# Kernel tuning notes

Hardware: AMD Instinct MI355X
Metric: run time of the kernel (lower is better)

## Reference

```python
import jax, jax.numpy as jnp
import numpy as np

BITS = (2, 4, 8)
GROUP = 4
EPS = 1e-5


def _ste_round(x):
    return x + jax.lax.stop_gradient(jnp.round(x) - x)


def _quant_act(x, b):
    s = float(2 ** b - 1)
    return _ste_round(jnp.clip(x, 0.0, 1.0) * s) / s


def _quant_weight(w, mean, std, b):
    # normalize by (mean, std) of the gating-selected channels, then b-bit uniform quant on [-1, 1]
    wn = jnp.clip((w - mean) / (std + EPS), -1.0, 1.0)
    s = float(2 ** b - 1)
    u = _ste_round((wn + 1.0) * 0.5 * s) / s
    return 2.0 * u - 1.0


def _mixed_qconv(x, w, w_mean, w_std, w_logits, a_logits):
    # bitwidth-selectable conv: softmax mixture over quantized weights / activations
    pw = jax.nn.softmax(w_logits)
    pa = jax.nn.softmax(a_logits)
    w_mix = sum(pw[i] * _quant_weight(w, w_mean, w_std, b) for i, b in enumerate(BITS))
    x_mix = sum(pa[i] * _quant_act(x, b) for i, b in enumerate(BITS))
    return jax.lax.conv_general_dilated(
        x_mix, w_mix, window_strides=(1, 1), padding='SAME',
        dimension_numbers=('NCHW', 'OIHW', 'NCHW'))


def _bn(x, g, b, m, v):
    inv = jax.lax.rsqrt(v + EPS)
    return (x - m[None, :, None, None]) * (g * inv)[None, :, None, None] + b[None, :, None, None]


def _masked_mean_std(w, mask):
    # mean/std over gate-selected filter slices; torch uses .data -> stop_gradient, unbiased std
    m = jnp.broadcast_to(mask, w.shape)
    cnt = jnp.sum(m)
    mean = jnp.sum(w * m) / cnt
    var = jnp.sum(m * (w - mean) ** 2) / (cnt - 1.0)
    return jax.lax.stop_gradient(mean), jax.lax.stop_gradient(jnp.sqrt(var))


def _indicator(w1, thr):
    n, c, h, wk = w1.shape
    fw = w1.reshape(n // GROUP, GROUP * c * h * wk)
    nf = fw / jnp.max(jnp.abs(fw))
    norm = jnp.sum(jnp.abs(nf), axis=1) / (GROUP * c * h * wk)  # [n_choices]
    soft = jax.nn.sigmoid(norm - thr)
    hard = (norm > thr).astype(w1.dtype)
    return hard - jax.lax.stop_gradient(soft) + soft  # STE indicator


def setup_inputs() -> dict:
    key = jax.random.key(0)
    ks = jax.random.split(key, 10)
    B, C, H, W = 64, 256, 32, 32
    return {
        'x': jax.random.normal(ks[0], (B, C, H, W), jnp.float32),
        'w1': jax.random.normal(ks[1], (C, C, 3, 3), jnp.float32) * 0.05,
        'w2': jax.random.normal(ks[2], (C, C, 3, 3), jnp.float32) * 0.05,
        'bn1_gamma': jnp.ones((C,), jnp.float32),
        'bn1_beta': jnp.zeros((C,), jnp.float32),
        'bn1_mean': jax.random.normal(ks[3], (C,), jnp.float32) * 0.1,
        'bn1_var': jax.random.uniform(ks[4], (C,), jnp.float32, 0.5, 1.5),
        'bn2_gamma': jnp.ones((C,), jnp.float32),
        'bn2_beta': jnp.zeros((C,), jnp.float32),
        'bn2_mean': jax.random.normal(ks[5], (C,), jnp.float32) * 0.1,
        'bn2_var': jax.random.uniform(ks[6], (C,), jnp.float32, 0.5, 1.5),
        'threshold': jnp.zeros((1,), jnp.float32),
        'w_logits1': jax.random.normal(ks[7], (3,), jnp.float32) * 0.1,
        'a_logits1': jax.random.normal(ks[8], (3,), jnp.float32) * 0.1,
        'w_logits2': jax.random.normal(ks[9], (3,), jnp.float32) * 0.1,
        'a_logits2': jnp.zeros((3,), jnp.float32),
    }


def reference(x, w1, w2, bn1_gamma, bn1_beta, bn1_mean, bn1_var,
              bn2_gamma, bn2_beta, bn2_mean, bn2_var, threshold,
              w_logits1, a_logits1, w_logits2, a_logits2):
    thr = threshold[0]
    ind = _indicator(w1, thr)                       # [n_choices]
    ind_ch = jnp.repeat(ind, GROUP)                 # [out_plane]
    gate_mask = jax.lax.stop_gradient((ind_ch > 0).astype(x.dtype))

    # both_preact path
    residual = x
    h = jax.nn.relu(_bn(x, bn1_gamma, bn1_beta, bn1_mean, bn1_var))
    m1, s1 = _masked_mean_std(w1, gate_mask[:, None, None, None])
    h = _mixed_qconv(h, w1, m1, s1, w_logits1, a_logits1)
    h = jax.nn.relu(_bn(h, bn2_gamma, bn2_beta, bn2_mean, bn2_var))
    m2, s2 = _masked_mean_std(w2, gate_mask[None, :, None, None])
    h = h * ind_ch[None, :, None, None]             # differentiable channel gating
    h = _mixed_qconv(h, w2, m2, s2, w_logits2, a_logits2)
    return h + residual
```

## Files before the change

kernel.cpp:

```cpp
#include <hip/hip_runtime.h>
#include <stdint.h>

#define EPSF 1e-5f

typedef _Float16 h8_t __attribute__((ext_vector_type(8)));
typedef float f4_t __attribute__((ext_vector_type(4)));

#define BB 64
#define CC 256
#define HH 32
#define WW 32
#define HP 34
#define WP 34
#define MTOT (BB*HH*WW)
#define WELEMS (CC*CC*9)
#define PADIMG (HP*WP*CC)
#define PADTOT (BB*PADIMG)

#define S_MAXABS 0
#define S_GSUM   1
#define S_SUM1   129
#define S_SQ1    130
#define S_SUM2   131
#define S_SQ2    132
#define S_M1     133
#define S_S1     134
#define S_M2     135
#define S_S2     136
#define S_PW1    137
#define S_PA1    140
#define S_PW2    143
#define S_PA2    146
#define S_INDCH  160
#define S_GATE   416
#define S_BN1SC  672
#define S_BN1SH  928
#define S_BN2SC  1184
#define S_BN2SH  1440

#define OFF_STATS 0
#define OFF_A1    8192
#define OFF_A2    (OFF_A1 + PADTOT*2)
#define OFF_W1T   (OFF_A2 + PADTOT*2)
#define OFF_W2T   (OFF_W1T + 9*CC*CC*2)

__device__ __forceinline__ void async_load16(void* lds, const void* g) {
  __builtin_amdgcn_global_load_lds(
      reinterpret_cast<uint32_t __attribute__((address_space(1)))*>((uintptr_t)g),
      reinterpret_cast<uint32_t __attribute__((address_space(3)))*>((uint32_t)(uintptr_t)lds),
      16, 0, 0);
}

__device__ __forceinline__ float wave_sum(float v) {
  for (int o = 32; o; o >>= 1) v += __shfl_down(v, o);
  return v;
}
__device__ __forceinline__ float wave_max(float v) {
  for (int o = 32; o; o >>= 1) v = fmaxf(v, __shfl_down(v, o));
  return v;
}

__global__ void k_groupstats(const float* __restrict__ w1, float* stats) {
  int g = blockIdx.x;
  const float* p = w1 + g * 9216;
  float s = 0.f, mx = 0.f;
  for (int i = threadIdx.x; i < 9216; i += 256) {
    float v = fabsf(p[i]);
    s += v; mx = fmaxf(mx, v);
  }
  s = wave_sum(s); mx = wave_max(mx);
  __shared__ float ls[4], lm[4];
  int lane = threadIdx.x & 63, w = threadIdx.x >> 6;
  if (lane == 0) { ls[w] = s; lm[w] = mx; }
  __syncthreads();
  if (threadIdx.x == 0) {
    float ss = ls[0] + ls[1] + ls[2] + ls[3];
    float mm = fmaxf(fmaxf(lm[0], lm[1]), fmaxf(lm[2], lm[3]));
    stats[S_GSUM + g] = ss;
    atomicMax((unsigned int*)(stats + S_MAXABS), __float_as_uint(mm));
  }
}

__device__ __forceinline__ void softmax3(const float* l, float* out) {
  float m = fmaxf(fmaxf(l[0], l[1]), l[2]);
  float e0 = expf(l[0] - m), e1 = expf(l[1] - m), e2 = expf(l[2] - m);
  float inv = 1.f / (e0 + e1 + e2);
  out[0] = e0 * inv; out[1] = e1 * inv; out[2] = e2 * inv;
}

__global__ void k_prep(const float* thr_p,
                       const float* bn1g, const float* bn1b, const float* bn1m, const float* bn1v,
                       const float* bn2g, const float* bn2b, const float* bn2m, const float* bn2v,
                       const float* wl1, const float* al1, const float* wl2, const float* al2,
                       float* stats) {
  int t = threadIdx.x;
  float thr = thr_p[0];
  float maxab = stats[S_MAXABS];
  __shared__ float ind[64];
  if (t < 64) {
    float norm = stats[S_GSUM + t] / maxab / 9216.0f;
    float soft = 1.f / (1.f + expf(-(norm - thr)));
    float hard = (norm > thr) ? 1.f : 0.f;
    ind[t] = (hard - soft) + soft;
  }
  __syncthreads();
  {
    float iv = ind[t >> 2];
    stats[S_INDCH + t] = iv;
    stats[S_GATE + t] = (iv > 0.f) ? 1.f : 0.f;
    float sc1 = bn1g[t] * (1.f / sqrtf(bn1v[t] + EPSF));
    stats[S_BN1SC + t] = sc1;
    stats[S_BN1SH + t] = bn1b[t] - bn1m[t] * sc1;
    float sc2 = bn2g[t] * (1.f / sqrtf(bn2v[t] + EPSF));
    stats[S_BN2SC + t] = sc2;
    stats[S_BN2SH + t] = bn2b[t] - bn2m[t] * sc2;
  }
  if (t == 0) {
    softmax3(wl1, stats + S_PW1);
    softmax3(al1, stats + S_PA1);
    softmax3(wl2, stats + S_PW2);
    softmax3(al2, stats + S_PA2);
  }
}

__global__ void k_masked(const float* __restrict__ w1, const float* __restrict__ w2,
                         float* stats) {
  const float* gate = stats + S_GATE;
  float s1 = 0.f, q1 = 0.f, s2 = 0.f, q2 = 0.f;
  for (int i = blockIdx.x * 256 + threadIdx.x; i < 2 * WELEMS; i += gridDim.x * 256) {
    if (i < WELEMS) {
      int o = i / 2304;
      float m = gate[o];
      float v = w1[i];
      s1 += m * v; q1 += m * v * v;
    } else {
      int j = i - WELEMS;
      int ic = (j / 9) & 255;
      float m = gate[ic];
      float v = w2[j];
      s2 += m * v; q2 += m * v * v;
    }
  }
  s1 = wave_sum(s1); q1 = wave_sum(q1); s2 = wave_sum(s2); q2 = wave_sum(q2);
  __shared__ float red[4][4];
  int lane = threadIdx.x & 63, w = threadIdx.x >> 6;
  if (lane == 0) { red[w][0] = s1; red[w][1] = q1; red[w][2] = s2; red[w][3] = q2; }
  __syncthreads();
  if (threadIdx.x == 0) {
    float a = 0, b = 0, c = 0, d = 0;
    for (int k = 0; k < 4; ++k) { a += red[k][0]; b += red[k][1]; c += red[k][2]; d += red[k][3]; }
    atomicAdd(stats + S_SUM1, a); atomicAdd(stats + S_SQ1, b);
    atomicAdd(stats + S_SUM2, c); atomicAdd(stats + S_SQ2, d);
  }
}

__global__ void k_final(float* stats) {
  int t = threadIdx.x;
  float g = stats[S_GATE + t];
  g = wave_sum(g);
  __shared__ float red[4];
  int lane = t & 63, w = t >> 6;
  if (lane == 0) red[w] = g;
  __syncthreads();
  if (t == 0) {
    float ns = red[0] + red[1] + red[2] + red[3];
    float cnt = ns * 2304.0f;
    float m1 = stats[S_SUM1] / cnt;
    float v1 = (stats[S_SQ1] - cnt * m1 * m1) / (cnt - 1.0f);
    stats[S_M1] = m1; stats[S_S1] = sqrtf(fmaxf(v1, 0.f));
    float m2 = stats[S_SUM2] / cnt;
    float v2 = (stats[S_SQ2] - cnt * m2 * m2) / (cnt - 1.0f);
    stats[S_M2] = m2; stats[S_S2] = sqrtf(fmaxf(v2, 0.f));
  }
}

__global__ void k_wprep(const float* __restrict__ w1, const float* __restrict__ w2,
                        const float* __restrict__ stats,
                        _Float16* __restrict__ wt1, _Float16* __restrict__ wt2) {
  int t = blockIdx.x * 256 + threadIdx.x;
  int which = (t >= WELEMS) ? 1 : 0;
  int r = which ? t - WELEMS : t;
  int e = r >> 16;
  int o = (r >> 8) & 255;
  int ci = r & 255;
  const float* w = which ? w2 : w1;
  float mean = stats[which ? S_M2 : S_M1];
  float sd = stats[which ? S_S2 : S_S1] + EPSF;
  const float* pw = stats + (which ? S_PW2 : S_PW1);
  float v = w[((o << 8) | ci) * 9 + e];
  float wn = fminf(fmaxf((v - mean) / sd, -1.f), 1.f);
  float u0 = rintf((wn + 1.f) * 0.5f * 3.f) / 3.f;
  float u1 = rintf((wn + 1.f) * 0.5f * 15.f) / 15.f;
  float u2 = rintf((wn + 1.f) * 0.5f * 255.f) / 255.f;
  float mix = pw[0] * (2.f * u0 - 1.f) + pw[1] * (2.f * u1 - 1.f) + pw[2] * (2.f * u2 - 1.f);
  (which ? wt2 : wt1)[r] = (_Float16)mix;
}

__global__ void k_borders(_Float16* a1, _Float16* a2) {
  int bid = blockIdx.x;
  _Float16* base = (bid >= BB * 132) ? a2 : a1;
  int r = (bid >= BB * 132) ? bid - BB * 132 : bid;
  int n = r / 132, b = r % 132;
  int yy, xx;
  if (b < 34)       { yy = 0;       xx = b; }
  else if (b < 68)  { yy = 33;      xx = b - 34; }
  else if (b < 100) { yy = b - 67;  xx = 0; }
  else              { yy = b - 99;  xx = 33; }
  uint64_t* p = (uint64_t*)(base + ((size_t)(n * HP + yy) * WP + xx) * CC);
  p[threadIdx.x] = 0ull;
}

#define APR_STRIDE 264
__global__ void k_aprep(const float* __restrict__ xin, const float* __restrict__ stats,
                        _Float16* __restrict__ a1) {
  __shared__ __attribute__((aligned(16))) _Float16 lds[32 * APR_STRIDE];
  int n = blockIdx.x >> 5, y = blockIdx.x & 31;
  int t = threadIdx.x;
  int x = t & 31, c0 = t >> 5;
  float pa0 = stats[S_PA1], pa1 = stats[S_PA1 + 1], pa2 = stats[S_PA1 + 2];
  const float* bsc = stats + S_BN1SC;
  const float* bsh = stats + S_BN1SH;
  for (int cc = 0; cc < 32; ++cc) {
    int c = cc * 8 + c0;
    float v = xin[((n * CC + c) * HH + y) * WW + x];
    v = fmaxf(v * bsc[c] + bsh[c], 0.f);
    float cl = fminf(v, 1.f);
    float q = pa0 * (rintf(cl * 3.f) / 3.f) + pa1 * (rintf(cl * 15.f) / 15.f)
            + pa2 * (rintf(cl * 255.f) / 255.f);
    lds[x * APR_STRIDE + c] = (_Float16)q;
  }
  __syncthreads();
  _Float16* orow = a1 + ((size_t)(n * HP + (y + 1)) * WP + 1) * CC;
  for (int it = 0; it < 4; ++it) {
    int qid = it * 256 + t;
    int xx = qid >> 5, c8 = (qid & 31) * 8;
    *(h8_t*)(orow + xx * CC + c8) = *(const h8_t*)(lds + xx * APR_STRIDE + c8);
  }
}

template <bool SW>
__global__ __launch_bounds__(256) void k_conv(
    const _Float16* __restrict__ act,
    const _Float16* __restrict__ wts,
    const float* __restrict__ stats,
    _Float16* __restrict__ a2out,
    const float* __restrict__ resid,
    float* __restrict__ out) {
  __shared__ __attribute__((aligned(16))) _Float16 As[128 * 64];
  __shared__ __attribute__((aligned(16))) _Float16 Ws[128 * 64];
  const int tid = threadIdx.x;
  const int lane = tid & 63, wid = tid >> 6;
  const int blk_co = blockIdx.x & 1;
  const int blk_m = blockIdx.x >> 1;

  const int srow = wid * 8 + (lane >> 3);
  const int g = (lane & 7) ^ (lane >> 3);
  int abase[4], wbase[4];
#pragma unroll
  for (int q = 0; q < 4; ++q) {
    int r = q * 32 + srow;
    int m = blk_m * 128 + r;
    int n = m >> 10, y = (m >> 5) & 31, x = m & 31;
    abase[q] = ((n * HP + y) * WP + x) * CC + g * 8;
    wbase[q] = (blk_co * 128 + r) * CC + g * 8;
  }

  const int wr = wid >> 1, wc = wid & 1;

  f4_t acc[4][4];
  const f4_t z4 = {0.f, 0.f, 0.f, 0.f};
#pragma unroll
  for (int i = 0; i < 4; ++i)
#pragma unroll
    for (int j = 0; j < 4; ++j) acc[i][j] = z4;

  int raoff[4], rboff[4];
#pragma unroll
  for (int i = 0; i < 4; ++i) {
    int ra = wr * 64 + i * 16 + (lane & 15);
    int sa = (lane >> 4) ^ (lane & 7);
    raoff[i] = ra * 64 + sa * 8;
    int rb = wc * 64 + i * 16 + (lane & 15);
    rboff[i] = rb * 64 + sa * 8;
  }

#pragma unroll 1
  for (int e = 0; e < 9; ++e) {
    const int kh = e / 3, kw = e - 3 * kh;
    const int aoffe = (kh * WP + kw) * CC;
    const int woffe = e * CC * CC;
#pragma unroll
    for (int kc = 0; kc < 4; ++kc) {
      const int ao = aoffe + kc * 64;
      const int wo = woffe + kc * 64;
      __syncthreads();
#pragma unroll
      for (int q = 0; q < 4; ++q) {
        async_load16(As + (q * 32 + wid * 8) * 64, act + abase[q] + ao);
        async_load16(Ws + (q * 32 + wid * 8) * 64, wts + wbase[q] + wo);
      }
      __syncthreads();
      const _Float16* aT = SW ? Ws : As;
      const _Float16* bT = SW ? As : Ws;
#pragma unroll
      for (int kk = 0; kk < 2; ++kk) {
        h8_t fa[4], fb[4];
#pragma unroll
        for (int i = 0; i < 4; ++i) {
          fa[i] = *(const h8_t*)(aT + (raoff[i] ^ (kk * 32)));
          fb[i] = *(const h8_t*)(bT + (rboff[i] ^ (kk * 32)));
        }
#pragma unroll
        for (int i = 0; i < 4; ++i)
#pragma unroll
          for (int j = 0; j < 4; ++j)
            acc[i][j] = __builtin_amdgcn_mfma_f32_16x16x32_f16(fa[i], fb[j], acc[i][j], 0, 0, 0);
      }
    }
  }

  const int quad = lane >> 4;
  const int cq = lane & 15;
  if (!SW) {
    const float pa0 = stats[S_PA2], pa1 = stats[S_PA2 + 1], pa2 = stats[S_PA2 + 2];
#pragma unroll
    for (int j = 0; j < 4; ++j) {
      const int co = blk_co * 128 + wc * 64 + j * 16 + cq;
      const float sc = stats[S_BN2SC + co];
      const float sh = stats[S_BN2SH + co];
      const float ic = stats[S_INDCH + co];
#pragma unroll
      for (int i = 0; i < 4; ++i) {
        const int mbase = blk_m * 128 + wr * 64 + i * 16 + quad * 4;
#pragma unroll
        for (int rg = 0; rg < 4; ++rg) {
          const int m = mbase + rg;
          const int n = m >> 10, y = (m >> 5) & 31, x = m & 31;
          float h = fmaxf(acc[i][j][rg] * sc + sh, 0.f) * ic;
          float cl = fminf(h, 1.f);
          float q = pa0 * (rintf(cl * 3.f) / 3.f) + pa1 * (rintf(cl * 15.f) / 15.f)
                  + pa2 * (rintf(cl * 255.f) / 255.f);
          a2out[((size_t)(n * HP + y + 1) * WP + (x + 1)) * CC + co] = (_Float16)q;
        }
      }
    }
  } else {
#pragma unroll
    for (int j = 0; j < 4; ++j) {
      const int m = blk_m * 128 + wc * 64 + j * 16 + cq;
      const int n = m >> 10, y = (m >> 5) & 31, x = m & 31;
#pragma unroll
      for (int i = 0; i < 4; ++i) {
        const int cobase = blk_co * 128 + wr * 64 + i * 16 + quad * 4;
#pragma unroll
        for (int rg = 0; rg < 4; ++rg) {
          const int co = cobase + rg;
          const int idx = ((n * CC + co) << 10) + (y << 5) + x;
          out[idx] = acc[i][j][rg] + resid[idx];
        }
      }
    }
  }
}

extern "C" void kernel_launch(void* const* d_in, const int* in_sizes, int n_in,
                              void* d_out, int out_size, void* d_ws, size_t ws_size,
                              hipStream_t stream) {
  const float* x    = (const float*)d_in[0];
  const float* w1   = (const float*)d_in[1];
  const float* w2   = (const float*)d_in[2];
  const float* bn1g = (const float*)d_in[3];
  const float* bn1b = (const float*)d_in[4];
  const float* bn1m = (const float*)d_in[5];
  const float* bn1v = (const float*)d_in[6];
  const float* bn2g = (const float*)d_in[7];
  const float* bn2b = (const float*)d_in[8];
  const float* bn2m = (const float*)d_in[9];
  const float* bn2v = (const float*)d_in[10];
  const float* thr  = (const float*)d_in[11];
  const float* wl1  = (const float*)d_in[12];
  const float* al1  = (const float*)d_in[13];
  const float* wl2  = (const float*)d_in[14];
  const float* al2  = (const float*)d_in[15];

  char* ws = (char*)d_ws;
  float* stats = (float*)(ws + OFF_STATS);
  _Float16* a1 = (_Float16*)(ws + OFF_A1);
  _Float16* a2 = (_Float16*)(ws + OFF_A2);
  _Float16* wt1 = (_Float16*)(ws + OFF_W1T);
  _Float16* wt2 = (_Float16*)(ws + OFF_W2T);
  float* out = (float*)d_out;

  hipMemsetAsync(stats, 0, 8192, stream);
  k_borders<<<2 * BB * 132, 64, 0, stream>>>(a1, a2);
  k_groupstats<<<64, 256, 0, stream>>>(w1, stats);
  k_prep<<<1, 256, 0, stream>>>(thr, bn1g, bn1b, bn1m, bn1v,
                                bn2g, bn2b, bn2m, bn2v, wl1, al1, wl2, al2, stats);
  k_masked<<<512, 256, 0, stream>>>(w1, w2, stats);
  k_final<<<1, 256, 0, stream>>>(stats);
  k_wprep<<<(2 * WELEMS) / 256, 256, 0, stream>>>(w1, w2, stats, wt1, wt2);
  k_aprep<<<BB * HH, 256, 0, stream>>>(x, stats, a1);
  k_conv<false><<<1024, 256, 0, stream>>>(a1, wt1, stats, a2, nullptr, nullptr);
  k_conv<true><<<1024, 256, 0, stream>>>(a2, wt2, stats, nullptr, x, out);
}
```

Measured before the change: 408.9 us.

## Fuse preprocessing kernels, precompute per-group weight stats, remap conv blocks per XCD

Merges the group-stats, masked-stats and finalize kernels into one per-group partial-sum pass plus a single prep kernel, so the gated mean/std comes from per-group sums instead of an atomic pass over all weights. It also removes the memset. Weight prep now works per output filter, staging results in LDS and writing 16-byte vectors. Activation prep uses float4 loads and takes over the border zeroing, which removes a separate kernel. The conv block index is remapped so consecutive M tiles land on the same XCD for L2 reuse.

```diff
diff --git a/kernel.cpp b/kernel.cpp
--- a/kernel.cpp
+++ b/kernel.cpp
@@ -17,26 +17,25 @@
 #define PADIMG (HP*WP*CC)
 #define PADTOT (BB*PADIMG)
 
-#define S_MAXABS 0
-#define S_GSUM   1
-#define S_SUM1   129
-#define S_SQ1    130
-#define S_SUM2   131
-#define S_SQ2    132
-#define S_M1     133
-#define S_S1     134
-#define S_M2     135
-#define S_S2     136
-#define S_PW1    137
-#define S_PA1    140
-#define S_PW2    143
-#define S_PA2    146
-#define S_INDCH  160
-#define S_GATE   416
-#define S_BN1SC  672
-#define S_BN1SH  928
-#define S_BN2SC  1184
-#define S_BN2SH  1440
+#define S_GSUM   0
+#define S_GMAX   64
+#define S_W1S    128
+#define S_W1Q    192
+#define S_W2S    256
+#define S_W2Q    320
+#define S_M1     384
+#define S_SD1    385
+#define S_M2     386
+#define S_SD2    387
+#define S_PW1    388
+#define S_PA1    391
+#define S_PW2    394
+#define S_PA2    397
+#define S_INDCH  400
+#define S_BN1SC  656
+#define S_BN1SH  912
+#define S_BN2SC  1168
+#define S_BN2SH  1424
 
 #define OFF_STATS 0
 #define OFF_A1    8192
@@ -60,27 +59,6 @@
   return v;
 }
 
-__global__ void k_groupstats(const float* __restrict__ w1, float* stats) {
-  int g = blockIdx.x;
-  const float* p = w1 + g * 9216;
-  float s = 0.f, mx = 0.f;
-  for (int i = threadIdx.x; i < 9216; i += 256) {
-    float v = fabsf(p[i]);
-    s += v; mx = fmaxf(mx, v);
-  }
-  s = wave_sum(s); mx = wave_max(mx);
-  __shared__ float ls[4], lm[4];
-  int lane = threadIdx.x & 63, w = threadIdx.x >> 6;
-  if (lane == 0) { ls[w] = s; lm[w] = mx; }
-  __syncthreads();
-  if (threadIdx.x == 0) {
-    float ss = ls[0] + ls[1] + ls[2] + ls[3];
-    float mm = fmaxf(fmaxf(lm[0], lm[1]), fmaxf(lm[2], lm[3]));
-    stats[S_GSUM + g] = ss;
-    atomicMax((unsigned int*)(stats + S_MAXABS), __float_as_uint(mm));
-  }
-}
-
 __device__ __forceinline__ void softmax3(const float* l, float* out) {
   float m = fmaxf(fmaxf(l[0], l[1]), l[2]);
   float e0 = expf(l[0] - m), e1 = expf(l[1] - m), e2 = expf(l[2] - m);
@@ -88,149 +66,183 @@
   out[0] = e0 * inv; out[1] = e1 * inv; out[2] = e2 * inv;
 }
 
-__global__ void k_prep(const float* thr_p,
-                       const float* bn1g, const float* bn1b, const float* bn1m, const float* bn1v,
-                       const float* bn2g, const float* bn2b, const float* bn2m, const float* bn2v,
-                       const float* wl1, const float* al1, const float* wl2, const float* al2,
-                       float* stats) {
+__global__ void k_stats(const float* __restrict__ w1, const float* __restrict__ w2,
+                        float* stats) {
+  __shared__ float red[4][4];
+  int bid = blockIdx.x, t = threadIdx.x;
+  int lane = t & 63, w = t >> 6;
+  if (bid < 64) {
+    const float* p = w1 + bid * 9216;
+    float sa = 0.f, s = 0.f, q = 0.f, mx = 0.f;
+    for (int i = t; i < 9216; i += 256) {
+      float v = p[i];
+      float a = fabsf(v);
+      sa += a; s += v; q += v * v; mx = fmaxf(mx, a);
+    }
+    sa = wave_sum(sa); s = wave_sum(s); q = wave_sum(q); mx = wave_max(mx);
+    if (lane == 0) { red[w][0] = sa; red[w][1] = s; red[w][2] = q; red[w][3] = mx; }
+    __syncthreads();
+    if (t == 0) {
+      float a = 0, b = 0, c = 0, d = 0;
+      for (int k = 0; k < 4; ++k) {
+        a += red[k][0]; b += red[k][1]; c += red[k][2]; d = fmaxf(d, red[k][3]);
+      }
+      stats[S_GSUM + bid] = a;
+      stats[S_W1S + bid] = b;
+      stats[S_W1Q + bid] = c;
+      stats[S_GMAX + bid] = d;
+    }
+  } else {
+    int g = bid - 64;
+    const float* p = w2 + (size_t)t * 2304 + g * 36;
+    float s = 0.f, q = 0.f;
+#pragma unroll
+    for (int i = 0; i < 36; ++i) { float v = p[i]; s += v; q += v * v; }
+    s = wave_sum(s); q = wave_sum(q);
+    if (lane == 0) { red[w][0] = s; red[w][1] = q; }
+    __syncthreads();
+    if (t == 0) {
+      float a = 0, b = 0;
+      for (int k = 0; k < 4; ++k) { a += red[k][0]; b += red[k][1]; }
+      stats[S_W2S + g] = a;
+      stats[S_W2Q + g] = b;
+    }
+  }
+}
+
+__global__ void k_prep2(const float* thr_p,
+                        const float* bn1g, const float* bn1b, const float* bn1m, const float* bn1v,
+                        const float* bn2g, const float* bn2b, const float* bn2m, const float* bn2v,
+                        const float* wl1, const float* al1, const float* wl2, const float* al2,
+                        float* stats) {
   int t = threadIdx.x;
-  float thr = thr_p[0];
-  float maxab = stats[S_MAXABS];
-  __shared__ float ind[64];
+  __shared__ float sind[64];
   if (t < 64) {
-    float norm = stats[S_GSUM + t] / maxab / 9216.0f;
+    float thr = thr_p[0];
+    float mx = wave_max(stats[S_GMAX + t]);
+    mx = __shfl(mx, 0);
+    float norm = stats[S_GSUM + t] / mx / 9216.0f;
     float soft = 1.f / (1.f + expf(-(norm - thr)));
     float hard = (norm > thr) ? 1.f : 0.f;
-    ind[t] = (hard - soft) + soft;
+    float iv = (hard - soft) + soft;
+    sind[t] = iv;
+    float gate = (iv > 0.f) ? 1.f : 0.f;
+    float ng = wave_sum(gate);
+    float s1 = wave_sum(gate * stats[S_W1S + t]);
+    float q1 = wave_sum(gate * stats[S_W1Q + t]);
+    float s2 = wave_sum(gate * stats[S_W2S + t]);
+    float q2 = wave_sum(gate * stats[S_W2Q + t]);
+    if (t == 0) {
+      float cnt = ng * 4.0f * 2304.0f;
+      float m1 = s1 / cnt;
+      float v1 = (q1 - cnt * m1 * m1) / (cnt - 1.0f);
+      stats[S_M1] = m1; stats[S_SD1] = sqrtf(fmaxf(v1, 0.f));
+      float m2 = s2 / cnt;
+      float v2 = (q2 - cnt * m2 * m2) / (cnt - 1.0f);
+      stats[S_M2] = m2; stats[S_SD2] = sqrtf(fmaxf(v2, 0.f));
+      softmax3(wl1, stats + S_PW1);
+      softmax3(al1, stats + S_PA1);
+      softmax3(wl2, stats + S_PW2);
+      softmax3(al2, stats + S_PA2);
+    }
   }
   __syncthreads();
-  {
-    float iv = ind[t >> 2];
-    stats[S_INDCH + t] = iv;
-    stats[S_GATE + t] = (iv > 0.f) ? 1.f : 0.f;
-    float sc1 = bn1g[t] * (1.f / sqrtf(bn1v[t] + EPSF));
-    stats[S_BN1SC + t] = sc1;
-    stats[S_BN1SH + t] = bn1b[t] - bn1m[t] * sc1;
-    float sc2 = bn2g[t] * (1.f / sqrtf(bn2v[t] + EPSF));
-    stats[S_BN2SC + t] = sc2;
-    stats[S_BN2SH + t] = bn2b[t] - bn2m[t] * sc2;
-  }
-  if (t == 0) {
-    softmax3(wl1, stats + S_PW1);
-    softmax3(al1, stats + S_PA1);
-    softmax3(wl2, stats + S_PW2);
-    softmax3(al2, stats + S_PA2);
-  }
-}
-
-__global__ void k_masked(const float* __restrict__ w1, const float* __restrict__ w2,
-                         float* stats) {
-  const float* gate = stats + S_GATE;
-  float s1 = 0.f, q1 = 0.f, s2 = 0.f, q2 = 0.f;
-  for (int i = blockIdx.x * 256 + threadIdx.x; i < 2 * WELEMS; i += gridDim.x * 256) {
-    if (i < WELEMS) {
-      int o = i / 2304;
-      float m = gate[o];
-      float v = w1[i];
-      s1 += m * v; q1 += m * v * v;
-    } else {
-      int j = i - WELEMS;
-      int ic = (j / 9) & 255;
-      float m = gate[ic];
-      float v = w2[j];
-      s2 += m * v; q2 += m * v * v;
-    }
-  }
-  s1 = wave_sum(s1); q1 = wave_sum(q1); s2 = wave_sum(s2); q2 = wave_sum(q2);
-  __shared__ float red[4][4];
-  int lane = threadIdx.x & 63, w = threadIdx.x >> 6;
-  if (lane == 0) { red[w][0] = s1; red[w][1] = q1; red[w][2] = s2; red[w][3] = q2; }
-  __syncthreads();
-  if (threadIdx.x == 0) {
-    float a = 0, b = 0, c = 0, d = 0;
-    for (int k = 0; k < 4; ++k) { a += red[k][0]; b += red[k][1]; c += red[k][2]; d += red[k][3]; }
-    atomicAdd(stats + S_SUM1, a); atomicAdd(stats + S_SQ1, b);
-    atomicAdd(stats + S_SUM2, c); atomicAdd(stats + S_SQ2, d);
-  }
-}
-
-__global__ void k_final(float* stats) {
-  int t = threadIdx.x;
-  float g = stats[S_GATE + t];
-  g = wave_sum(g);
-  __shared__ float red[4];
-  int lane = t & 63, w = t >> 6;
-  if (lane == 0) red[w] = g;
-  __syncthreads();
-  if (t == 0) {
-    float ns = red[0] + red[1] + red[2] + red[3];
-    float cnt = ns * 2304.0f;
-    float m1 = stats[S_SUM1] / cnt;
-    float v1 = (stats[S_SQ1] - cnt * m1 * m1) / (cnt - 1.0f);
-    stats[S_M1] = m1; stats[S_S1] = sqrtf(fmaxf(v1, 0.f));
-    float m2 = stats[S_SUM2] / cnt;
-    float v2 = (stats[S_SQ2] - cnt * m2 * m2) / (cnt - 1.0f);
-    stats[S_M2] = m2; stats[S_S2] = sqrtf(fmaxf(v2, 0.f));
-  }
-}
-
+  stats[S_INDCH + t] = sind[t >> 2];
+  float sc1 = bn1g[t] * (1.f / sqrtf(bn1v[t] + EPSF));
+  stats[S_BN1SC + t] = sc1;
+  stats[S_BN1SH + t] = bn1b[t] - bn1m[t] * sc1;
+  float sc2 = bn2g[t] * (1.f / sqrtf(bn2v[t] + EPSF));
+  stats[S_BN2SC + t] = sc2;
+  stats[S_BN2SH + t] = bn2b[t] - bn2m[t] * sc2;
+}
+
+#define WPS 264
 __global__ void k_wprep(const float* __restrict__ w1, const float* __restrict__ w2,
                         const float* __restrict__ stats,
                         _Float16* __restrict__ wt1, _Float16* __restrict__ wt2) {
-  int t = blockIdx.x * 256 + threadIdx.x;
-  int which = (t >= WELEMS) ? 1 : 0;
-  int r = which ? t - WELEMS : t;
-  int e = r >> 16;
-  int o = (r >> 8) & 255;
-  int ci = r & 255;
-  const float* w = which ? w2 : w1;
+  __shared__ __attribute__((aligned(16))) _Float16 lds[9 * WPS];
+  int bid = blockIdx.x;
+  int which = bid >> 8, o = bid & 255;
+  const float* w = (which ? w2 : w1) + (size_t)o * 2304;
   float mean = stats[which ? S_M2 : S_M1];
-  float sd = stats[which ? S_S2 : S_S1] + EPSF;
+  float sd = stats[which ? S_SD2 : S_SD1] + EPSF;
   const float* pw = stats + (which ? S_PW2 : S_PW1);
-  float v = w[((o << 8) | ci) * 9 + e];
-  float wn = fminf(fmaxf((v - mean) / sd, -1.f), 1.f);
-  float u0 = rintf((wn + 1.f) * 0.5f * 3.f) / 3.f;
-  float u1 = rintf((wn + 1.f) * 0.5f * 15.f) / 15.f;
-  float u2 = rintf((wn + 1.f) * 0.5f * 255.f) / 255.f;
-  float mix = pw[0] * (2.f * u0 - 1.f) + pw[1] * (2.f * u1 - 1.f) + pw[2] * (2.f * u2 - 1.f);
-  (which ? wt2 : wt1)[r] = (_Float16)mix;
-}
-
-__global__ void k_borders(_Float16* a1, _Float16* a2) {
-  int bid = blockIdx.x;
-  _Float16* base = (bid >= BB * 132) ? a2 : a1;
-  int r = (bid >= BB * 132) ? bid - BB * 132 : bid;
-  int n = r / 132, b = r % 132;
-  int yy, xx;
-  if (b < 34)       { yy = 0;       xx = b; }
-  else if (b < 68)  { yy = 33;      xx = b - 34; }
-  else if (b < 100) { yy = b - 67;  xx = 0; }
-  else              { yy = b - 99;  xx = 33; }
-  uint64_t* p = (uint64_t*)(base + ((size_t)(n * HP + yy) * WP + xx) * CC);
-  p[threadIdx.x] = 0ull;
+  float p0 = pw[0], p1 = pw[1], p2 = pw[2];
+  int t = threadIdx.x;
+#pragma unroll
+  for (int it = 0; it < 9; ++it) {
+    int f = it * 256 + t;
+    float v = w[f];
+    float wn = fminf(fmaxf((v - mean) / sd, -1.f), 1.f);
+    float u0 = rintf((wn + 1.f) * 0.5f * 3.f) / 3.f;
+    float u1 = rintf((wn + 1.f) * 0.5f * 15.f) / 15.f;
+    float u2 = rintf((wn + 1.f) * 0.5f * 255.f) / 255.f;
+    float mix = p0 * (2.f * u0 - 1.f) + p1 * (2.f * u1 - 1.f) + p2 * (2.f * u2 - 1.f);
+    int ci = f / 9;
+    int e = f - 9 * ci;
+    lds[e * WPS + ci] = (_Float16)mix;
+  }
+  __syncthreads();
+  _Float16* dst0 = (which ? wt2 : wt1) + o * 256;
+#pragma unroll
+  for (int it = 0; it < 2; ++it) {
+    int qid = it * 256 + t;
+    if (qid < 288) {
+      int e = qid >> 5, c8 = (qid & 31) * 8;
+      *(h8_t*)(dst0 + e * 65536 + c8) = *(const h8_t*)(lds + e * WPS + c8);
+    }
+  }
 }
 
 #define APR_STRIDE 264
 __global__ void k_aprep(const float* __restrict__ xin, const float* __restrict__ stats,
-                        _Float16* __restrict__ a1) {
+                        _Float16* __restrict__ a1, _Float16* __restrict__ a2) {
   __shared__ __attribute__((aligned(16))) _Float16 lds[32 * APR_STRIDE];
-  int n = blockIdx.x >> 5, y = blockIdx.x & 31;
+  int bid = blockIdx.x;
   int t = threadIdx.x;
-  int x = t & 31, c0 = t >> 5;
+  if (bid >= BB * HH) {
+    int b = bid - BB * HH;
+    _Float16* img = (b >= BB ? a2 : a1) + (size_t)(b & 63) * PADIMG;
+    uint64_t* u = (uint64_t*)img;
+#pragma unroll
+    for (int it = 0; it < 17; ++it) {
+      int idx = it * 256 + t;
+      int r33 = (idx >= 2176);
+      u[(size_t)(r33 ? 33 * WP * 64 : 0) + (idx - (r33 ? 2176 : 0))] = 0ull;
+    }
+#pragma unroll
+    for (int it = 0; it < 16; ++it) {
+      int idx = it * 256 + t;
+      int p = idx >> 6;
+      int y = 1 + (p >> 1), x = (p & 1) ? 33 : 0;
+      u[(size_t)(y * WP + x) * 64 + (idx & 63)] = 0ull;
+    }
+    return;
+  }
+  int n = bid >> 5, y = bid & 31;
+  int x4 = (t & 7) * 4, c0 = t >> 3;
   float pa0 = stats[S_PA1], pa1 = stats[S_PA1 + 1], pa2 = stats[S_PA1 + 2];
   const float* bsc = stats + S_BN1SC;
   const float* bsh = stats + S_BN1SH;
-  for (int cc = 0; cc < 32; ++cc) {
-    int c = cc * 8 + c0;
-    float v = xin[((n * CC + c) * HH + y) * WW + x];
-    v = fmaxf(v * bsc[c] + bsh[c], 0.f);
-    float cl = fminf(v, 1.f);
-    float q = pa0 * (rintf(cl * 3.f) / 3.f) + pa1 * (rintf(cl * 15.f) / 15.f)
-            + pa2 * (rintf(cl * 255.f) / 255.f);
-    lds[x * APR_STRIDE + c] = (_Float16)q;
+#pragma unroll
+  for (int it = 0; it < 8; ++it) {
+    int c = it * 32 + c0;
+    const float* src = xin + ((size_t)(n * CC + c) * HH + y) * WW + x4;
+    float4 v = *(const float4*)src;
+    float sc = bsc[c], sh = bsh[c];
+#pragma unroll
+    for (int k = 0; k < 4; ++k) {
+      float vv = (&v.x)[k];
+      vv = fmaxf(vv * sc + sh, 0.f);
+      float cl = fminf(vv, 1.f);
+      float q = pa0 * (rintf(cl * 3.f) / 3.f) + pa1 * (rintf(cl * 15.f) / 15.f)
+              + pa2 * (rintf(cl * 255.f) / 255.f);
+      lds[(x4 + k) * APR_STRIDE + c] = (_Float16)q;
+    }
   }
   __syncthreads();
   _Float16* orow = a1 + ((size_t)(n * HP + (y + 1)) * WP + 1) * CC;
+#pragma unroll
   for (int it = 0; it < 4; ++it) {
     int qid = it * 256 + t;
     int xx = qid >> 5, c8 = (qid & 31) * 8;
@@ -250,8 +262,10 @@
   __shared__ __attribute__((aligned(16))) _Float16 Ws[128 * 64];
   const int tid = threadIdx.x;
   const int lane = tid & 63, wid = tid >> 6;
-  const int blk_co = blockIdx.x & 1;
-  const int blk_m = blockIdx.x >> 1;
+  const int xcd = blockIdx.x & 7;
+  const int j = blockIdx.x >> 3;
+  const int blk_co = j >> 6;
+  const int blk_m = xcd * 64 + (j & 63);
 
   const int srow = wid * 8 + (lane >> 3);
   const int g = (lane & 7) ^ (lane >> 3);
@@ -272,7 +286,7 @@
 #pragma unroll
   for (int i = 0; i < 4; ++i)
 #pragma unroll
-    for (int j = 0; j < 4; ++j) acc[i][j] = z4;
+    for (int j2 = 0; j2 < 4; ++j2) acc[i][j2] = z4;
 
   int raoff[4], rboff[4];
 #pragma unroll
@@ -313,8 +327,8 @@
 #pragma unroll
         for (int i = 0; i < 4; ++i)
 #pragma unroll
-          for (int j = 0; j < 4; ++j)
-            acc[i][j] = __builtin_amdgcn_mfma_f32_16x16x32_f16(fa[i], fb[j], acc[i][j], 0, 0, 0);
+          for (int j2 = 0; j2 < 4; ++j2)
+            acc[i][j2] = __builtin_amdgcn_mfma_f32_16x16x32_f16(fa[i], fb[j2], acc[i][j2], 0, 0, 0);
       }
     }
   }
@@ -324,8 +338,8 @@
   if (!SW) {
     const float pa0 = stats[S_PA2], pa1 = stats[S_PA2 + 1], pa2 = stats[S_PA2 + 2];
 #pragma unroll
-    for (int j = 0; j < 4; ++j) {
-      const int co = blk_co * 128 + wc * 64 + j * 16 + cq;
+    for (int j2 = 0; j2 < 4; ++j2) {
+      const int co = blk_co * 128 + wc * 64 + j2 * 16 + cq;
       const float sc = stats[S_BN2SC + co];
       const float sh = stats[S_BN2SH + co];
       const float ic = stats[S_INDCH + co];
@@ -336,7 +350,7 @@
         for (int rg = 0; rg < 4; ++rg) {
           const int m = mbase + rg;
           const int n = m >> 10, y = (m >> 5) & 31, x = m & 31;
-          float h = fmaxf(acc[i][j][rg] * sc + sh, 0.f) * ic;
+          float h = fmaxf(acc[i][j2][rg] * sc + sh, 0.f) * ic;
           float cl = fminf(h, 1.f);
           float q = pa0 * (rintf(cl * 3.f) / 3.f) + pa1 * (rintf(cl * 15.f) / 15.f)
                   + pa2 * (rintf(cl * 255.f) / 255.f);
@@ -346,8 +360,8 @@
     }
   } else {
 #pragma unroll
-    for (int j = 0; j < 4; ++j) {
-      const int m = blk_m * 128 + wc * 64 + j * 16 + cq;
+    for (int j2 = 0; j2 < 4; ++j2) {
+      const int m = blk_m * 128 + wc * 64 + j2 * 16 + cq;
       const int n = m >> 10, y = (m >> 5) & 31, x = m & 31;
 #pragma unroll
       for (int i = 0; i < 4; ++i) {
@@ -356,7 +370,7 @@
         for (int rg = 0; rg < 4; ++rg) {
           const int co = cobase + rg;
           const int idx = ((n * CC + co) << 10) + (y << 5) + x;
-          out[idx] = acc[i][j][rg] + resid[idx];
+          out[idx] = acc[i][j2][rg] + resid[idx];
         }
       }
     }
@@ -391,15 +405,11 @@
   _Float16* wt2 = (_Float16*)(ws + OFF_W2T);
   float* out = (float*)d_out;
 
-  hipMemsetAsync(stats, 0, 8192, stream);
-  k_borders<<<2 * BB * 132, 64, 0, stream>>>(a1, a2);
-  k_groupstats<<<64, 256, 0, stream>>>(w1, stats);
-  k_prep<<<1, 256, 0, stream>>>(thr, bn1g, bn1b, bn1m, bn1v,
-                                bn2g, bn2b, bn2m, bn2v, wl1, al1, wl2, al2, stats);
-  k_masked<<<512, 256, 0, stream>>>(w1, w2, stats);
-  k_final<<<1, 256, 0, stream>>>(stats);
-  k_wprep<<<(2 * WELEMS) / 256, 256, 0, stream>>>(w1, w2, stats, wt1, wt2);
-  k_aprep<<<BB * HH, 256, 0, stream>>>(x, stats, a1);
+  k_stats<<<128, 256, 0, stream>>>(w1, w2, stats);
+  k_prep2<<<1, 256, 0, stream>>>(thr, bn1g, bn1b, bn1m, bn1v,
+                                 bn2g, bn2b, bn2m, bn2v, wl1, al1, wl2, al2, stats);
+  k_wprep<<<512, 256, 0, stream>>>(w1, w2, stats, wt1, wt2);
+  k_aprep<<<BB * HH + 128, 256, 0, stream>>>(x, stats, a1, a2);
   k_conv<false><<<1024, 256, 0, stream>>>(a1, wt1, stats, a2, nullptr, nullptr);
   k_conv<true><<<1024, 256, 0, stream>>>(a2, wt2, stats, nullptr, x, out);
 }
```

Result: faster. 363.8 us (-11.0%).
